# Kernel optimization log

Hardware: AMD Instinct MI355X
Metric: run time of the kernel (lower is better)

The kernel has to match this reference:

```python
import jax, jax.numpy as jnp
import numpy as np

DIM = 512
NUM_HEADS = 8
HEAD_DIM = DIM // NUM_HEADS
B, S = 2, 2048


def setup_inputs() -> dict:
    key = jax.random.key(0)
    ks = jax.random.split(key, 16)
    scale = 1.0 / np.sqrt(DIM)
    inp = {
        "x": jax.random.normal(ks[0], (B, S, DIM), dtype=jnp.float32),
        "Qexpl": jax.random.normal(ks[1], (B, S, DIM), dtype=jnp.float32),
        "Kexpl": jax.random.normal(ks[2], (B, S, DIM), dtype=jnp.float32),
        "fl": jax.random.uniform(ks[3], (B,), dtype=jnp.float32),
        "fu": jax.random.uniform(ks[4], (B,), dtype=jnp.float32),
        "age": jax.random.uniform(ks[5], (B,), dtype=jnp.float32),
        "gender": jax.random.uniform(ks[6], (B,), dtype=jnp.float32),
        # Linear params: weight stored as [out, in] like torch; y = x @ W.T + b
        "Wq": jax.random.normal(ks[7], (DIM, DIM), dtype=jnp.float32) * scale,
        "bq": jnp.zeros((DIM,), dtype=jnp.float32),
        "Wk": jax.random.normal(ks[8], (DIM, DIM), dtype=jnp.float32) * scale,
        "bk": jnp.zeros((DIM,), dtype=jnp.float32),
        "Wv": jax.random.normal(ks[9], (DIM, DIM), dtype=jnp.float32) * scale,
        "bv": jnp.zeros((DIM,), dtype=jnp.float32),
        "Wo": jax.random.normal(ks[10], (DIM, DIM), dtype=jnp.float32) * scale,
        "bo": jnp.zeros((DIM,), dtype=jnp.float32),
    }
    return inp


def reference(x, Qexpl, Kexpl, fl, fu, age, gender, Wq, bq, Wk, bk, Wv, bv, Wo, bo):
    # drofe_fn is None -> Q/K projections used directly.
    Q = Qexpl @ Wq.T + bq            # [B, S, D]
    K = Kexpl @ Wk.T + bk            # [B, S, D]
    V = x @ Wv.T + bv                # [B, S, D]

    def split_heads(t):  # [B, S, D] -> [B, H, S, hd]
        return t.reshape(B, S, NUM_HEADS, HEAD_DIM).transpose(0, 2, 1, 3)

    Qh, Kh, Vh = split_heads(Q), split_heads(K), split_heads(V)
    scale = 1.0 / np.sqrt(HEAD_DIM).astype(np.float32)
    scores = jnp.einsum("bhqd,bhkd->bhqk", Qh, Kh) * scale  # [B, H, S, S]
    weights = jax.nn.softmax(scores, axis=-1)
    attn = jnp.einsum("bhqk,bhkd->bhqd", weights, Vh)        # [B, H, S, hd]
    attn = attn.transpose(0, 2, 1, 3).reshape(B, S, DIM)
    return attn @ Wo.T + bo
```

## Files before the change

### kernel.cpp

```cpp
#include <hip/hip_runtime.h>
#include <hip/hip_bf16.h>

typedef unsigned short ushort_t;
typedef __attribute__((ext_vector_type(8))) short bf16x8;
typedef __attribute__((ext_vector_type(4))) float f32x4;

__device__ __forceinline__ ushort_t f2bf(float f) {
    union { float f; unsigned u; } v; v.f = f;
    unsigned r = v.u + 0x7FFF + ((v.u >> 16) & 1);
    return (ushort_t)(r >> 16);
}
__device__ __forceinline__ bf16x8 ld8(const ushort_t* p) { return *(const bf16x8*)p; }

__device__ __forceinline__ unsigned cvt2(float x, float y) {
    __hip_bfloat162 h = __float22bfloat162_rn(make_float2(x, y));
    unsigned r; __builtin_memcpy(&r, &h, 4); return r;
}
__device__ __forceinline__ bf16x8 pack8f(float4 a, float4 b) {
    union { unsigned u[4]; bf16x8 v; } o;
    o.u[0] = cvt2(a.x, a.y); o.u[1] = cvt2(a.z, a.w);
    o.u[2] = cvt2(b.x, b.y); o.u[3] = cvt2(b.z, b.w);
    return o.v;
}

__device__ __forceinline__ void gload_lds16(const ushort_t* g, ushort_t* l) {
    __builtin_amdgcn_global_load_lds(
        (const __attribute__((address_space(1))) void*)g,
        (__attribute__((address_space(3))) void*)l, 16, 0, 0);
}

__global__ __launch_bounds__(256, 2)
void proj_qkv_kernel(const float* __restrict__ Qe, const float* __restrict__ Ke,
                     const float* __restrict__ x,
                     const float* __restrict__ Wq, const float* __restrict__ Wk,
                     const float* __restrict__ Wv,
                     const float* __restrict__ bq, const float* __restrict__ bk,
                     const float* __restrict__ bv,
                     ushort_t* __restrict__ Qo, ushort_t* __restrict__ Ko,
                     ushort_t* __restrict__ Vt)
{
    __shared__ ushort_t smem[2 * 128 * 72];
    ushort_t* lA = smem;
    ushort_t* lB = smem + 128 * 72;

    const int z = blockIdx.z;
    const float* A = (z == 0) ? Qe : (z == 1) ? Ke : x;
    const float* W = (z == 0) ? Wq : (z == 1) ? Wk : Wv;
    const float* bias = (z == 0) ? bq : (z == 1) ? bk : bv;

    const int m0 = blockIdx.y * 128, n0 = blockIdx.x * 128;
    const int t = threadIdx.x;
    const int lane = t & 63, wave = t >> 6;
    const int wm = (wave & 1) * 64, wn = (wave >> 1) * 64;
    const int fr = lane & 15, quad = lane >> 4;

    f32x4 acc[4][4] = {};
    float4 fa[4][2], fw[4][2];

#pragma unroll
    for (int i = 0; i < 4; ++i) {
        int s = i * 256 + t;
        int r = s >> 3, jp = s & 7;
        const float* pa = A + (size_t)(m0 + r) * 512 + jp * 8;
        fa[i][0] = *(const float4*)pa; fa[i][1] = *(const float4*)(pa + 4);
        const float* pw = W + (size_t)(n0 + r) * 512 + jp * 8;
        fw[i][0] = *(const float4*)pw; fw[i][1] = *(const float4*)(pw + 4);
    }

    for (int kk = 0; kk < 8; ++kk) {
        if (kk) __syncthreads();
#pragma unroll
        for (int i = 0; i < 4; ++i) {
            int s = i * 256 + t;
            int r = s >> 3, jp = s & 7;
            *(bf16x8*)(lA + r * 72 + jp * 8) = pack8f(fa[i][0], fa[i][1]);
            *(bf16x8*)(lB + r * 72 + jp * 8) = pack8f(fw[i][0], fw[i][1]);
        }
        __syncthreads();
        if (kk < 7) {
            int k0 = (kk + 1) * 64;
#pragma unroll
            for (int i = 0; i < 4; ++i) {
                int s = i * 256 + t;
                int r = s >> 3, jp = s & 7;
                const float* pa = A + (size_t)(m0 + r) * 512 + k0 + jp * 8;
                fa[i][0] = *(const float4*)pa; fa[i][1] = *(const float4*)(pa + 4);
                const float* pw = W + (size_t)(n0 + r) * 512 + k0 + jp * 8;
                fw[i][0] = *(const float4*)pw; fw[i][1] = *(const float4*)(pw + 4);
            }
        }

#pragma unroll
        for (int ks = 0; ks < 2; ++ks) {
            bf16x8 af[4], bfrag[4];
#pragma unroll
            for (int mt = 0; mt < 4; ++mt)
                af[mt] = ld8(lA + (wm + mt * 16 + fr) * 72 + (ks * 4 + quad) * 8);
#pragma unroll
            for (int nt = 0; nt < 4; ++nt)
                bfrag[nt] = ld8(lB + (wn + nt * 16 + fr) * 72 + (ks * 4 + quad) * 8);
#pragma unroll
            for (int mt = 0; mt < 4; ++mt)
#pragma unroll
                for (int nt = 0; nt < 4; ++nt)
                    acc[mt][nt] = __builtin_amdgcn_mfma_f32_16x16x32_bf16(
                        af[mt], bfrag[nt], acc[mt][nt], 0, 0, 0);
        }
    }

    const float C1 = 0.125f * 1.44269504088896340736f;
    if (z != 2) {
        ushort_t* dst = (z == 0) ? Qo : Ko;
#pragma unroll
        for (int nt = 0; nt < 4; ++nt) {
            int n = n0 + wn + nt * 16 + fr;
            float bb = bias[n];
#pragma unroll
            for (int mt = 0; mt < 4; ++mt) {
                int mb = m0 + wm + mt * 16 + quad * 4;
                if (z == 0) {
#pragma unroll
                    for (int r = 0; r < 4; ++r)
                        dst[(size_t)(mb + r) * 512 + n] = f2bf((acc[mt][nt][r] + bb) * C1);
                } else {
#pragma unroll
                    for (int r = 0; r < 4; ++r)
                        dst[(size_t)(mb + r) * 512 + n] = f2bf(acc[mt][nt][r] + bb);
                }
            }
        }
    } else {
        __syncthreads();
        ushort_t* lT = smem;
#pragma unroll
        for (int nt = 0; nt < 4; ++nt) {
            int nl = wn + nt * 16 + fr;
            float bb = bias[n0 + nl];
#pragma unroll
            for (int mt = 0; mt < 4; ++mt) {
                int tm = wm + mt * 16 + quad * 4;
#pragma unroll
                for (int r = 0; r < 4; ++r) {
                    int tl = tm + r;
                    int sg = 8 * (tl & 15) + ((tl >> 4) & 7);
                    lT[nl * 136 + sg] = f2bf(acc[mt][nt][r] + bb);
                }
            }
        }
        __syncthreads();
        const int bidx = m0 >> 11, m0t = m0 & 2047;
#pragma unroll
        for (int i = 0; i < 8; ++i) {
            int s = i * 256 + t;
            int row = s >> 4, c = s & 15;
            int n = n0 + row;
            int h = n >> 6, d = n & 63;
            bf16x8 v = ld8(lT + row * 136 + c * 8);
            *(bf16x8*)(Vt + ((size_t)((bidx * 8 + h) * 64 + d)) * 2048 + m0t + c * 8) = v;
        }
    }
}

__global__ __launch_bounds__(256, 2)
void gemm_o_kernel(const ushort_t* __restrict__ A, const float* __restrict__ W,
                   const float* __restrict__ bias, float* __restrict__ dst)
{
    __shared__ ushort_t lA[64 * 72];
    __shared__ ushort_t lB[64 * 72];
    const int m0 = blockIdx.y * 64, n0 = blockIdx.x * 64;
    const int t = threadIdx.x;
    const int lane = t & 63, wave = t >> 6;
    const int wm = (wave & 1) * 32, wn = (wave >> 1) * 32;
    const int fr = lane & 15, quad = lane >> 4;

    f32x4 acc[2][2] = {};
    bf16x8 va[2];
    float4 fw[2][2];

#pragma unroll
    for (int i = 0; i < 2; ++i) {
        int s = i * 256 + t;
        int r = s >> 3, jp = s & 7;
        va[i] = ld8(A + (size_t)(m0 + r) * 512 + jp * 8);
        const float* p = W + (size_t)(n0 + r) * 512 + jp * 8;
        fw[i][0] = *(const float4*)p; fw[i][1] = *(const float4*)(p + 4);
    }

    for (int kk = 0; kk < 8; ++kk) {
        if (kk) __syncthreads();
#pragma unroll
        for (int i = 0; i < 2; ++i) {
            int s = i * 256 + t;
            int r = s >> 3, jp = s & 7;
            *(bf16x8*)(lA + r * 72 + jp * 8) = va[i];
            *(bf16x8*)(lB + r * 72 + jp * 8) = pack8f(fw[i][0], fw[i][1]);
        }
        __syncthreads();
        if (kk < 7) {
            int k0 = (kk + 1) * 64;
#pragma unroll
            for (int i = 0; i < 2; ++i) {
                int s = i * 256 + t;
                int r = s >> 3, jp = s & 7;
                va[i] = ld8(A + (size_t)(m0 + r) * 512 + k0 + jp * 8);
                const float* p = W + (size_t)(n0 + r) * 512 + k0 + jp * 8;
                fw[i][0] = *(const float4*)p; fw[i][1] = *(const float4*)(p + 4);
            }
        }

        bf16x8 af[2][2], bfrag[2][2];
#pragma unroll
        for (int ks = 0; ks < 2; ++ks) {
#pragma unroll
            for (int mt = 0; mt < 2; ++mt)
                af[mt][ks] = ld8(lA + (wm + mt * 16 + fr) * 72 + (ks * 4 + quad) * 8);
#pragma unroll
            for (int nt = 0; nt < 2; ++nt)
                bfrag[nt][ks] = ld8(lB + (wn + nt * 16 + fr) * 72 + (ks * 4 + quad) * 8);
        }
#pragma unroll
        for (int ks = 0; ks < 2; ++ks)
#pragma unroll
            for (int mt = 0; mt < 2; ++mt)
#pragma unroll
                for (int nt = 0; nt < 2; ++nt)
                    acc[mt][nt] = __builtin_amdgcn_mfma_f32_16x16x32_bf16(
                        af[mt][ks], bfrag[nt][ks], acc[mt][nt], 0, 0, 0);
    }

#pragma unroll
    for (int nt = 0; nt < 2; ++nt) {
        int n = n0 + wn + nt * 16 + fr;
        float bb = bias[n];
#pragma unroll
        for (int mt = 0; mt < 2; ++mt) {
            int mb = m0 + wm + mt * 16 + quad * 4;
#pragma unroll
            for (int r = 0; r < 4; ++r)
                dst[(size_t)(mb + r) * 512 + n] = acc[mt][nt][r] + bb;
        }
    }
}

__global__ __launch_bounds__(256, 2)
void attn_kernel(const ushort_t* __restrict__ Q, const ushort_t* __restrict__ K,
                 const ushort_t* __restrict__ Vt, ushort_t* __restrict__ O)
{
    __shared__ ushort_t lK[2 * 128 * 64];
    __shared__ ushort_t lV[64 * 128];
    __shared__ ushort_t lP[64 * 128];

    const int b = blockIdx.z, h = blockIdx.y;
    const int q0 = blockIdx.x * 64;
    const int t = threadIdx.x;
    const int lane = t & 63, w = t >> 6;
    const int wq = w * 16;
    const int fr = lane & 15, quad = lane >> 4;
    const int fr7 = fr & 7;

    bf16x8 aq[2];
    {
        const ushort_t* qp = Q + (size_t)(b * 2048 + q0 + wq + fr) * 512 + h * 64 + quad * 8;
        aq[0] = ld8(qp);
        aq[1] = ld8(qp + 32);
    }

    const int krl = lane >> 3;
    const ushort_t* kbase = K + (size_t)(b * 2048 + w * 32 + krl) * 512 + h * 64
                              + (((lane & 7) ^ (krl & 7)) << 3);
    const int vrl = w * 4 + (lane >> 4);
    const ushort_t* vbase = Vt + (size_t)((b * 8 + h) * 64 + vrl) * 2048
                              + (((lane & 15) ^ (vrl & 7)) << 3);

#pragma unroll
    for (int i = 0; i < 4; ++i)
        gload_lds16(kbase + (size_t)(i * 8) * 512, lK + (w * 32 + i * 8) * 64);
    __syncthreads();

    f32x4 oacc[4] = {};
    float lpart[4] = {};

    for (int tt = 0; tt < 16; ++tt) {
        const int kv = tt << 7;
        ushort_t* lKc = lK + ((tt & 1) << 13);
        ushort_t* lKn = lK + (((tt & 1) ^ 1) << 13);

#pragma unroll
        for (int i = 0; i < 4; ++i)
            gload_lds16(vbase + kv + (size_t)(i * 16) * 2048, lV + (i * 16 + w * 4) * 128);
        if (tt < 15) {
#pragma unroll
            for (int i = 0; i < 4; ++i)
                gload_lds16(kbase + (size_t)(kv + 128 + i * 8) * 512,
                            lKn + (w * 32 + i * 8) * 64);
        }

        f32x4 sc[8] = {};
#pragma unroll
        for (int ks = 0; ks < 2; ++ks)
#pragma unroll
            for (int nt = 0; nt < 8; ++nt) {
                bf16x8 kb = ld8(lKc + (nt * 16 + fr) * 64 + (((ks * 4 + quad) ^ fr7) << 3));
                sc[nt] = __builtin_amdgcn_mfma_f32_16x16x32_bf16(aq[ks], kb, sc[nt], 0, 0, 0);
            }

#pragma unroll
        for (int r = 0; r < 4; ++r) {
            int row = wq + quad * 4 + r;
            float pv[8]; float acc = 0.f;
#pragma unroll
            for (int nt = 0; nt < 8; ++nt) { pv[nt] = exp2f(sc[nt][r]); acc += pv[nt]; }
            lpart[r] += acc;
            union { unsigned u[4]; bf16x8 v; } pu;
            pu.u[0] = cvt2(pv[0], pv[1]); pu.u[1] = cvt2(pv[2], pv[3]);
            pu.u[2] = cvt2(pv[4], pv[5]); pu.u[3] = cvt2(pv[6], pv[7]);
            *(bf16x8*)(lP + row * 128 + ((fr ^ (row & 7)) << 3)) = pu.v;
        }

        if (tt < 15) asm volatile("s_waitcnt vmcnt(4)" ::: "memory");
        else         asm volatile("s_waitcnt vmcnt(0)" ::: "memory");
        __builtin_amdgcn_s_barrier();
        __builtin_amdgcn_sched_barrier(0);

#pragma unroll
        for (int ks = 0; ks < 4; ++ks) {
            int cs = ((ks * 4 + quad) ^ fr7) << 3;
            bf16x8 ap = ld8(lP + (wq + fr) * 128 + cs);
#pragma unroll
            for (int nt = 0; nt < 4; ++nt) {
                bf16x8 vb = ld8(lV + (nt * 16 + fr) * 128 + cs);
                oacc[nt] = __builtin_amdgcn_mfma_f32_16x16x32_bf16(ap, vb, oacc[nt], 0, 0, 0);
            }
        }
        __syncthreads();
    }

#pragma unroll
    for (int r = 0; r < 4; ++r) {
        float rs = lpart[r];
#pragma unroll
        for (int o = 1; o < 16; o <<= 1)
            rs += __shfl_xor(rs, o, 64);
        float inv = 1.f / rs;
        int q = q0 + wq + quad * 4 + r;
#pragma unroll
        for (int nt = 0; nt < 4; ++nt) {
            int d = nt * 16 + fr;
            O[(size_t)(b * 2048 + q) * 512 + h * 64 + d] = f2bf(oacc[nt][r] * inv);
        }
    }
}

extern "C" void kernel_launch(void* const* d_in, const int* in_sizes, int n_in,
                              void* d_out, int out_size, void* d_ws, size_t ws_size,
                              hipStream_t stream) {
    const float* x   = (const float*)d_in[0];
    const float* Qe  = (const float*)d_in[1];
    const float* Ke  = (const float*)d_in[2];
    const float* Wq  = (const float*)d_in[7];
    const float* bq  = (const float*)d_in[8];
    const float* Wk  = (const float*)d_in[9];
    const float* bk  = (const float*)d_in[10];
    const float* Wv  = (const float*)d_in[11];
    const float* bv  = (const float*)d_in[12];
    const float* Wo  = (const float*)d_in[13];
    const float* bo  = (const float*)d_in[14];

    const size_t NTOK = 2 * 2048;
    const size_t ACT = NTOK * 512;

    ushort_t* p = (ushort_t*)d_ws;
    ushort_t* Qws = p; p += ACT;
    ushort_t* Kws = p; p += ACT;
    ushort_t* Vt  = p; p += ACT;
    ushort_t* Ows = p; p += ACT;

    proj_qkv_kernel<<<dim3(4, 32, 3), 256, 0, stream>>>(Qe, Ke, x, Wq, Wk, Wv,
                                                        bq, bk, bv, Qws, Kws, Vt);
    attn_kernel<<<dim3(32, 8, 2), 256, 0, stream>>>(Qws, Kws, Vt, Ows);
    gemm_o_kernel<<<dim3(8, 64), 256, 0, stream>>>(Ows, Wo, bo, (float*)d_out);
}
```

Baseline: 165.3 us.

## Split attention KV range across two blocks and merge partial outputs

```diff
diff --git a/kernel.cpp b/kernel.cpp
--- a/kernel.cpp
+++ b/kernel.cpp
@@ -242,16 +242,19 @@
     }
 }
 
-__global__ __launch_bounds__(256, 2)
+__global__ __launch_bounds__(256, 3)
 void attn_kernel(const ushort_t* __restrict__ Q, const ushort_t* __restrict__ K,
-                 const ushort_t* __restrict__ Vt, ushort_t* __restrict__ O)
+                 const ushort_t* __restrict__ Vt, float* __restrict__ Opart,
+                 float* __restrict__ Lsum)
 {
-    __shared__ ushort_t lK[2 * 128 * 64];
+    __shared__ ushort_t lK[128 * 64];
     __shared__ ushort_t lV[64 * 128];
     __shared__ ushort_t lP[64 * 128];
 
-    const int b = blockIdx.z, h = blockIdx.y;
+    const int b = blockIdx.z >> 1, half = blockIdx.z & 1;
+    const int h = blockIdx.y;
     const int q0 = blockIdx.x * 64;
+    const int kvbase = half * 1024;
     const int t = threadIdx.x;
     const int lane = t & 63, w = t >> 6;
     const int wq = w * 16;
@@ -265,48 +268,72 @@
         aq[1] = ld8(qp + 32);
     }
 
-    const int krl = lane >> 3;
-    const ushort_t* kbase = K + (size_t)(b * 2048 + w * 32 + krl) * 512 + h * 64
-                              + (((lane & 7) ^ (krl & 7)) << 3);
+    const int krl = w * 32 + (lane >> 3);
+    const ushort_t* kg = K + (size_t)(b * 2048 + kvbase + krl) * 512 + h * 64
+                           + (lane & 7) * 8;
+    ushort_t* lk_wr = lK + krl * 64 + (((lane & 7) ^ (krl & 7)) << 3);
+
     const int vrl = w * 4 + (lane >> 4);
-    const ushort_t* vbase = Vt + (size_t)((b * 8 + h) * 64 + vrl) * 2048
+    const ushort_t* vbase = Vt + (size_t)((b * 8 + h) * 64 + vrl) * 2048 + kvbase
                               + (((lane & 15) ^ (vrl & 7)) << 3);
 
+    const ushort_t* kr0 = lK + fr * 64 + ((quad ^ fr7) << 3);
+    const ushort_t* kr1 = lK + fr * 64 + (((4 + quad) ^ fr7) << 3);
+    const ushort_t* vr[4];
+    const ushort_t* pr[4];
+#pragma unroll
+    for (int ks = 0; ks < 4; ++ks) {
+        int cs = (((ks * 4 + quad) ^ fr7) << 3);
+        vr[ks] = lV + fr * 128 + cs;
+        pr[ks] = lP + (wq + fr) * 128 + cs;
+    }
+    ushort_t* pw[4];
+#pragma unroll
+    for (int r = 0; r < 4; ++r) {
+        int row = wq + quad * 4 + r;
+        pw[r] = lP + row * 128 + ((fr ^ (row & 7)) << 3);
+    }
+
+    bf16x8 kreg[4];
 #pragma unroll
     for (int i = 0; i < 4; ++i)
-        gload_lds16(kbase + (size_t)(i * 8) * 512, lK + (w * 32 + i * 8) * 64);
+        kreg[i] = ld8(kg + (size_t)(i * 8) * 512);
+#pragma unroll
+    for (int i = 0; i < 4; ++i)
+        *(bf16x8*)(lk_wr + i * 8 * 64) = kreg[i];
     __syncthreads();
 
     f32x4 oacc[4] = {};
     float lpart[4] = {};
 
-    for (int tt = 0; tt < 16; ++tt) {
+    for (int tt = 0; tt < 8; ++tt) {
         const int kv = tt << 7;
-        ushort_t* lKc = lK + ((tt & 1) << 13);
-        ushort_t* lKn = lK + (((tt & 1) ^ 1) << 13);
 
 #pragma unroll
         for (int i = 0; i < 4; ++i)
             gload_lds16(vbase + kv + (size_t)(i * 16) * 2048, lV + (i * 16 + w * 4) * 128);
-        if (tt < 15) {
+        __builtin_amdgcn_sched_barrier(0);
+        if (tt < 7) {
 #pragma unroll
             for (int i = 0; i < 4; ++i)
-                gload_lds16(kbase + (size_t)(kv + 128 + i * 8) * 512,
-                            lKn + (w * 32 + i * 8) * 64);
-        }
+                kreg[i] = ld8(kg + (size_t)(kv + 128 + i * 8) * 512);
+        }
+        __builtin_amdgcn_sched_barrier(0);
 
         f32x4 sc[8] = {};
 #pragma unroll
-        for (int ks = 0; ks < 2; ++ks)
-#pragma unroll
-            for (int nt = 0; nt < 8; ++nt) {
-                bf16x8 kb = ld8(lKc + (nt * 16 + fr) * 64 + (((ks * 4 + quad) ^ fr7) << 3));
-                sc[nt] = __builtin_amdgcn_mfma_f32_16x16x32_bf16(aq[ks], kb, sc[nt], 0, 0, 0);
-            }
+        for (int nt = 0; nt < 8; ++nt) {
+            bf16x8 kb = ld8(kr0 + nt * 16 * 64);
+            sc[nt] = __builtin_amdgcn_mfma_f32_16x16x32_bf16(aq[0], kb, sc[nt], 0, 0, 0);
+        }
+#pragma unroll
+        for (int nt = 0; nt < 8; ++nt) {
+            bf16x8 kb = ld8(kr1 + nt * 16 * 64);
+            sc[nt] = __builtin_amdgcn_mfma_f32_16x16x32_bf16(aq[1], kb, sc[nt], 0, 0, 0);
+        }
 
 #pragma unroll
         for (int r = 0; r < 4; ++r) {
-            int row = wq + quad * 4 + r;
             float pv[8]; float acc = 0.f;
 #pragma unroll
             for (int nt = 0; nt < 8; ++nt) { pv[nt] = exp2f(sc[nt][r]); acc += pv[nt]; }
@@ -314,21 +341,26 @@
             union { unsigned u[4]; bf16x8 v; } pu;
             pu.u[0] = cvt2(pv[0], pv[1]); pu.u[1] = cvt2(pv[2], pv[3]);
             pu.u[2] = cvt2(pv[4], pv[5]); pu.u[3] = cvt2(pv[6], pv[7]);
-            *(bf16x8*)(lP + row * 128 + ((fr ^ (row & 7)) << 3)) = pu.v;
-        }
-
-        if (tt < 15) asm volatile("s_waitcnt vmcnt(4)" ::: "memory");
-        else         asm volatile("s_waitcnt vmcnt(0)" ::: "memory");
+            *(bf16x8*)pw[r] = pu.v;
+        }
+
+        if (tt < 7) asm volatile("s_waitcnt vmcnt(4)" ::: "memory");
+        else        asm volatile("s_waitcnt vmcnt(0)" ::: "memory");
         __builtin_amdgcn_s_barrier();
         __builtin_amdgcn_sched_barrier(0);
 
+        if (tt < 7) {
+#pragma unroll
+            for (int i = 0; i < 4; ++i)
+                *(bf16x8*)(lk_wr + i * 8 * 64) = kreg[i];
+        }
+
 #pragma unroll
         for (int ks = 0; ks < 4; ++ks) {
-            int cs = ((ks * 4 + quad) ^ fr7) << 3;
-            bf16x8 ap = ld8(lP + (wq + fr) * 128 + cs);
+            bf16x8 ap = ld8(pr[ks]);
 #pragma unroll
             for (int nt = 0; nt < 4; ++nt) {
-                bf16x8 vb = ld8(lV + (nt * 16 + fr) * 128 + cs);
+                bf16x8 vb = ld8(vr[ks] + nt * 16 * 128);
                 oacc[nt] = __builtin_amdgcn_mfma_f32_16x16x32_bf16(ap, vb, oacc[nt], 0, 0, 0);
             }
         }
@@ -341,14 +373,36 @@
 #pragma unroll
         for (int o = 1; o < 16; o <<= 1)
             rs += __shfl_xor(rs, o, 64);
-        float inv = 1.f / rs;
-        int q = q0 + wq + quad * 4 + r;
-#pragma unroll
-        for (int nt = 0; nt < 4; ++nt) {
-            int d = nt * 16 + fr;
-            O[(size_t)(b * 2048 + q) * 512 + h * 64 + d] = f2bf(oacc[nt][r] * inv);
-        }
-    }
+        int qrow = q0 + wq + quad * 4 + r;
+        float* od = Opart + ((size_t)(half * 2 + b) * 2048 + qrow) * 512 + h * 64;
+#pragma unroll
+        for (int nt = 0; nt < 4; ++nt)
+            od[nt * 16 + fr] = oacc[nt][r];
+        if (fr == 0)
+            Lsum[((half * 2 + b) * 8 + h) * 2048 + qrow] = rs;
+    }
+}
+
+__global__ __launch_bounds__(256)
+void merge_kernel(const float* __restrict__ Opart, const float* __restrict__ Lsum,
+                  ushort_t* __restrict__ Ows)
+{
+    int gid = blockIdx.x * 256 + threadIdx.x;
+    int row = gid >> 7;
+    int c4 = (gid & 127) << 2;
+    int b = row >> 11, q = row & 2047;
+    int h = c4 >> 6;
+    float l0 = Lsum[(b * 8 + h) * 2048 + q];
+    float l1 = Lsum[((2 + b) * 8 + h) * 2048 + q];
+    float inv = 1.f / (l0 + l1);
+    float4 o0 = *(const float4*)(Opart + (size_t)row * 512 + c4);
+    float4 o1 = *(const float4*)(Opart + (size_t)(row + 4096) * 512 + c4);
+    union { unsigned u[2]; } o;
+    o.u[0] = cvt2((o0.x + o1.x) * inv, (o0.y + o1.y) * inv);
+    o.u[1] = cvt2((o0.z + o1.z) * inv, (o0.w + o1.w) * inv);
+    unsigned* dst = (unsigned*)(Ows + (size_t)row * 512 + c4);
+    dst[0] = o.u[0];
+    dst[1] = o.u[1];
 }
 
 extern "C" void kernel_launch(void* const* d_in, const int* in_sizes, int n_in,
@@ -374,9 +428,12 @@
     ushort_t* Kws = p; p += ACT;
     ushort_t* Vt  = p; p += ACT;
     ushort_t* Ows = p; p += ACT;
+    float* Opart = (float*)p;
+    float* Lsum  = Opart + 2 * ACT;
 
     proj_qkv_kernel<<<dim3(4, 32, 3), 256, 0, stream>>>(Qe, Ke, x, Wq, Wk, Wv,
                                                         bq, bk, bv, Qws, Kws, Vt);
-    attn_kernel<<<dim3(32, 8, 2), 256, 0, stream>>>(Qws, Kws, Vt, Ows);
+    attn_kernel<<<dim3(32, 8, 4), 256, 0, stream>>>(Qws, Kws, Vt, Opart, Lsum);
+    merge_kernel<<<dim3(2048), 256, 0, stream>>>(Opart, Lsum, Ows);
     gemm_o_kernel<<<dim3(8, 64), 256, 0, stream>>>(Ows, Wo, bo, (float*)d_out);
 }
```

After: 168.4 us. No clear change (+1.8%).
